# Performance work log

Hardware: AMD Instinct MI355X
Metric: run time of the kernel (lower is better)

Reference implementation:

```python
import jax, jax.numpy as jnp
import numpy as np

S_STATES, C_TYPES, G_GENES = 16, 64, 20000


def setup_inputs() -> dict:
    key = jax.random.key(0)
    k1, k2, k3, k4 = jax.random.split(key, 4)
    Z_mu = jax.random.normal(k1, (C_TYPES, G_GENES), dtype=jnp.float32)
    # positive log-normal sigmas, moderate scale for numerical stability
    Z_sigma = jax.random.uniform(k2, (C_TYPES, G_GENES), dtype=jnp.float32) * 0.5 + 0.1
    # build a valid correlation matrix (PSD with unit diagonal) so var >= 0
    L = jax.random.normal(k3, (C_TYPES, C_TYPES), dtype=jnp.float32)
    cov = L @ L.T + C_TYPES * jnp.eye(C_TYPES, dtype=jnp.float32)
    d = jnp.sqrt(jnp.diag(cov))
    corr = cov / (d[:, None] * d[None, :])
    # cell_prob rows on the simplex (Dirichlet-like), per state
    cell_prob = jax.nn.softmax(jax.random.normal(k4, (S_STATES, C_TYPES), dtype=jnp.float32), axis=1)
    return {"Z_mu": Z_mu, "Z_sigma": Z_sigma, "corr": corr, "cell_prob": cell_prob}


def reference(Z_mu, Z_sigma, corr, cell_prob):
    """Vectorized LogNorm.calculate_mu_sigma.

    Z_mu, Z_sigma: (C, G); corr: (C, C); cell_prob: (S, C).
    Returns mu, sigma of shape (S, G) -- moment-matched log-normal sum params
    for every (state, gene) pair, matching the nested-loop torch original.
    """
    # EV[s,c,g] = exp(mu + sigma^2/2) * w  (first moment of each component, weighted)
    ev_base = jnp.exp(Z_mu + 0.5 * Z_sigma ** 2)            # (C, G)
    EV = cell_prob[:, :, None] * ev_base[None, :, :]         # (S, C, G)
    Ssum = EV.sum(axis=1)                                    # (S, G)
    # A[s,c,g] = EV * sigma; var = sum_{c,d} A_c corr_{cd} A_d / Ssum^2
    A = EV * Z_sigma[None, :, :]                             # (S, C, G)
    var = jnp.einsum('scg,cd,sdg->sg', A, corr, A) / (Ssum ** 2)  # (S, G)
    mu_s = jnp.log(Ssum) - 0.5 * var
    sigma_s = jnp.sqrt(var)
    return (mu_s, sigma_s)
```

## Files before the change

### kernel.cpp

```cpp
#include <hip/hip_runtime.h>


#define S_STATES 16
#define C_TYPES  64
#define G_GENES  20000
#define OUT_HALF (S_STATES * G_GENES)
#define NPAIR    96
#define PER_WAVE 24

typedef _Float16 f16x2 __attribute__((ext_vector_type(2)));
typedef _Float16 f16x8 __attribute__((ext_vector_type(8)));
typedef float    f32x4 __attribute__((ext_vector_type(4)));

union Frag8 { f16x2 p[4]; f16x8 v; uint4 u; _Float16 h[8]; };

__global__ __launch_bounds__(64)
void build_A(const float* __restrict__ corr, const float* __restrict__ w,
             unsigned short* __restrict__ cwA)
{
    const int p    = blockIdx.x;
    const int lane = threadIdx.x;
    const int gl   = lane & 15;
    const int q    = lane >> 4;
    Frag8 v;
    if (p < NPAIR) {
        const int dh = (p >= 64);
        const int c  = dh ? p - 32 : p;
        const int d0 = dh * 32 + q * 8;
        const float wc = w[gl * C_TYPES + c];
        const float4 c0 = *(const float4*)(corr + c * C_TYPES + d0);
        const float4 c1 = *(const float4*)(corr + c * C_TYPES + d0 + 4);
        const float4 w0 = *(const float4*)(w + gl * C_TYPES + d0);
        const float4 w1 = *(const float4*)(w + gl * C_TYPES + d0 + 4);
        const float cv[8] = {c0.x,c0.y,c0.z,c0.w,c1.x,c1.y,c1.z,c1.w};
        const float wv[8] = {w0.x,w0.y,w0.z,w0.w,w1.x,w1.y,w1.z,w1.w};
#pragma unroll
        for (int j = 0; j < 8; ++j) {
            const int d = d0 + j;
            const float sc = (d < c) ? 2.0f : (d == c ? 1.0f : 0.0f);
            v.h[j] = (_Float16)(sc * cv[j] * wc * wv[j]);
        }
    } else {
        const int k0 = (p - NPAIR) * 32 + q * 8;
        const float4 w0 = *(const float4*)(w + gl * C_TYPES + k0);
        const float4 w1 = *(const float4*)(w + gl * C_TYPES + k0 + 4);
        const float wv[8] = {w0.x,w0.y,w0.z,w0.w,w1.x,w1.y,w1.z,w1.w};
#pragma unroll
        for (int j = 0; j < 8; ++j) v.h[j] = (_Float16)wv[j];
    }
    *(uint4*)(cwA + (p << 9) + lane * 8) = v.u;
}

__global__ __launch_bounds__(256, 4)
void lognorm_main(const float* __restrict__ Z_mu,
                  const float* __restrict__ Z_sigma,
                  const unsigned short* __restrict__ cwA,
                  float* __restrict__ out)
{
    __shared__ f16x2 x2pT[16][35];
    __shared__ f16x2 x1pT[16][35];
    __shared__ float accs[4][S_STATES][17];
    __shared__ float ssum_s[S_STATES][17];

    const int gt    = blockIdx.x;
    const int tid   = threadIdx.x;
    const int w     = tid >> 6;
    const int lane  = tid & 63;
    const int gl    = lane & 15;
    const int q     = lane >> 4;
    const int gbase = gt * 16;

    Frag8 wf0, wf1;
    if (w == 0) {
        wf0.u = *(const uint4*)(cwA + ((NPAIR + 0) << 9) + lane * 8);
        wf1.u = *(const uint4*)(cwA + ((NPAIR + 1) << 9) + lane * 8);
    }

    {
        const int gx  = tid & 15;
        const int dpA = tid >> 4;
#pragma unroll
        for (int t = 0; t < 2; ++t) {
            const int dp = dpA + 16 * t;
            const float m0 = Z_mu   [(2*dp)     * G_GENES + gbase + gx];
            const float m1 = Z_mu   [(2*dp + 1) * G_GENES + gbase + gx];
            const float s0 = Z_sigma[(2*dp)     * G_GENES + gbase + gx];
            const float s1 = Z_sigma[(2*dp + 1) * G_GENES + gbase + gx];
            const float e0 = __expf(fmaf(0.5f * s0, s0, m0)) * 0.25f;
            const float e1 = __expf(fmaf(0.5f * s1, s1, m1)) * 0.25f;
            f16x2 a, b;
            a.x = (_Float16)(e0 * s0); a.y = (_Float16)(e1 * s1);
            b.x = (_Float16)e0;        b.y = (_Float16)e1;
            x2pT[gx][dp] = a;
            x1pT[gx][dp] = b;
        }
    }
    __syncthreads();

    f16x2 xh[2][4];
#pragma unroll
    for (int dh = 0; dh < 2; ++dh)
#pragma unroll
        for (int jp = 0; jp < 4; ++jp)
            xh[dh][jp] = x2pT[gl][dh * 16 + q * 4 + jp];

    const unsigned short* Abase = cwA + (w << 9) + lane * 8;
    const int wq = w >> 1;
    const int wc = w & 1;
    f32x4 acc0 = {0.f,0.f,0.f,0.f}, acc1 = {0.f,0.f,0.f,0.f};
#pragma unroll
    for (int i = 0; i < PER_WAVE; ++i) {
        Frag8 af; af.u = *(const uint4*)(Abase + (i << 11));
        const int dh = (i >= 16) ? 1 : 0;
        const int dp = 2*i - dh*16 + wq;
        const f16x2 pr = x2pT[gl][dp];
        const _Float16 xc = wc ? pr.y : pr.x;
        f16x2 s; s.x = xc; s.y = xc;
        Frag8 b;
#pragma unroll
        for (int jp = 0; jp < 4; ++jp) b.p[jp] = s * xh[dh][jp];
        if (i & 1) acc1 = __builtin_amdgcn_mfma_f32_16x16x32_f16(af.v, b.v, acc1, 0, 0, 0);
        else       acc0 = __builtin_amdgcn_mfma_f32_16x16x32_f16(af.v, b.v, acc0, 0, 0, 0);
    }
    const f32x4 acc = acc0 + acc1;
#pragma unroll
    for (int r = 0; r < 4; ++r) accs[w][q*4 + r][gl] = acc[r];

    if (w == 0) {
        Frag8 x1f0, x1f1;
#pragma unroll
        for (int jp = 0; jp < 4; ++jp) {
            x1f0.p[jp] = x1pT[gl][q*4 + jp];
            x1f1.p[jp] = x1pT[gl][16 + q*4 + jp];
        }
        f32x4 sa = {0.f,0.f,0.f,0.f};
        sa = __builtin_amdgcn_mfma_f32_16x16x32_f16(wf0.v, x1f0.v, sa, 0, 0, 0);
        sa = __builtin_amdgcn_mfma_f32_16x16x32_f16(wf1.v, x1f1.v, sa, 0, 0, 0);
#pragma unroll
        for (int r = 0; r < 4; ++r) ssum_s[q*4 + r][gl] = sa[r];
    }
    __syncthreads();

    const int s  = tid >> 4;
    const int gx = tid & 15;
    const float vn = (accs[0][s][gx] + accs[1][s][gx])
                   + (accs[2][s][gx] + accs[3][s][gx]);
    const float ss   = ssum_s[s][gx];
    const float rvar = fmaxf(vn, 0.f) / (ss * ss);
    out[s * G_GENES + gbase + gx] =
        __logf(ss) + 1.3862943611f - 0.5f * rvar;
    out[OUT_HALF + s * G_GENES + gbase + gx] = sqrtf(rvar);
}

extern "C" void kernel_launch(void* const* d_in, const int* in_sizes, int n_in,
                              void* d_out, int out_size, void* d_ws, size_t ws_size,
                              hipStream_t stream) {
    const float* Z_mu      = (const float*)d_in[0];
    const float* Z_sigma   = (const float*)d_in[1];
    const float* corr      = (const float*)d_in[2];
    const float* cell_prob = (const float*)d_in[3];
    float* out = (float*)d_out;
    unsigned short* cwA = (unsigned short*)d_ws;

    build_A<<<dim3(NPAIR + 2), dim3(64), 0, stream>>>(corr, cell_prob, cwA);

    const int gtiles = G_GENES / 16;
    lognorm_main<<<dim3(gtiles), dim3(256), 0, stream>>>(
        Z_mu, Z_sigma, cwA, out);
}
```

Before: 16.82 us.

## Widen gene tile to 64 per block with 16 waves reusing A fragments

```diff
diff --git a/kernel.cpp b/kernel.cpp
--- a/kernel.cpp
+++ b/kernel.cpp
@@ -6,7 +6,6 @@
 #define G_GENES  20000
 #define OUT_HALF (S_STATES * G_GENES)
 #define NPAIR    96
-#define PER_WAVE 24
 
 typedef _Float16 f16x2 __attribute__((ext_vector_type(2)));
 typedef _Float16 f16x8 __attribute__((ext_vector_type(8)));
@@ -51,16 +50,17 @@
     *(uint4*)(cwA + (p << 9) + lane * 8) = v.u;
 }
 
-__global__ __launch_bounds__(256, 4)
+__global__ __launch_bounds__(1024, 4)
 void lognorm_main(const float* __restrict__ Z_mu,
                   const float* __restrict__ Z_sigma,
                   const unsigned short* __restrict__ cwA,
                   float* __restrict__ out)
 {
-    __shared__ f16x2 x2pT[16][35];
-    __shared__ f16x2 x1pT[16][35];
-    __shared__ float accs[4][S_STATES][17];
-    __shared__ float ssum_s[S_STATES][17];
+    __shared__ f16x2   x2pT[64][33];
+    __shared__ f16x2   x1pT[64][33];
+    __shared__ _Float16 x2g[64][72];
+    __shared__ float   accs[16][S_STATES][66];
+    __shared__ float   ssum_s[S_STATES][66];
 
     const int gt    = blockIdx.x;
     const int tid   = threadIdx.x;
@@ -68,83 +68,96 @@
     const int lane  = tid & 63;
     const int gl    = lane & 15;
     const int q     = lane >> 4;
-    const int gbase = gt * 16;
-
-    Frag8 wf0, wf1;
-    if (w == 0) {
-        wf0.u = *(const uint4*)(cwA + ((NPAIR + 0) << 9) + lane * 8);
-        wf1.u = *(const uint4*)(cwA + ((NPAIR + 1) << 9) + lane * 8);
-    }
+    const int gbase = (gt < 312) ? gt * 64 : (G_GENES - 64);
 
     {
-        const int gx  = tid & 15;
-        const int dpA = tid >> 4;
-#pragma unroll
-        for (int t = 0; t < 2; ++t) {
-            const int dp = dpA + 16 * t;
-            const float m0 = Z_mu   [(2*dp)     * G_GENES + gbase + gx];
-            const float m1 = Z_mu   [(2*dp + 1) * G_GENES + gbase + gx];
-            const float s0 = Z_sigma[(2*dp)     * G_GENES + gbase + gx];
-            const float s1 = Z_sigma[(2*dp + 1) * G_GENES + gbase + gx];
-            const float e0 = __expf(fmaf(0.5f * s0, s0, m0)) * 0.25f;
-            const float e1 = __expf(fmaf(0.5f * s1, s1, m1)) * 0.25f;
-            f16x2 a, b;
-            a.x = (_Float16)(e0 * s0); a.y = (_Float16)(e1 * s1);
-            b.x = (_Float16)e0;        b.y = (_Float16)e1;
-            x2pT[gx][dp] = a;
-            x1pT[gx][dp] = b;
-        }
+        const int dp = tid >> 5;
+        const int ga = (tid & 31) * 2;
+        const float* zm = Z_mu    + (2*dp) * G_GENES + gbase + ga;
+        const float* zs = Z_sigma + (2*dp) * G_GENES + gbase + ga;
+        const float2 m0 = *(const float2*)zm;
+        const float2 m1 = *(const float2*)(zm + G_GENES);
+        const float2 s0 = *(const float2*)zs;
+        const float2 s1 = *(const float2*)(zs + G_GENES);
+        const float e00 = __expf(fmaf(0.5f*s0.x, s0.x, m0.x)) * 0.25f;
+        const float e01 = __expf(fmaf(0.5f*s0.y, s0.y, m0.y)) * 0.25f;
+        const float e10 = __expf(fmaf(0.5f*s1.x, s1.x, m1.x)) * 0.25f;
+        const float e11 = __expf(fmaf(0.5f*s1.y, s1.y, m1.y)) * 0.25f;
+        const float x200 = e00*s0.x, x201 = e01*s0.y;
+        const float x210 = e10*s1.x, x211 = e11*s1.y;
+        f16x2 a0; a0.x = (_Float16)x200; a0.y = (_Float16)x210;
+        f16x2 a1; a1.x = (_Float16)x201; a1.y = (_Float16)x211;
+        f16x2 b0; b0.x = (_Float16)e00;  b0.y = (_Float16)e10;
+        f16x2 b1; b1.x = (_Float16)e01;  b1.y = (_Float16)e11;
+        x2pT[ga][dp]   = a0;  x2pT[ga+1][dp] = a1;
+        x1pT[ga][dp]   = b0;  x1pT[ga+1][dp] = b1;
+        x2g[2*dp][ga]     = (_Float16)x200;  x2g[2*dp][ga+1]   = (_Float16)x201;
+        x2g[2*dp+1][ga]   = (_Float16)x210;  x2g[2*dp+1][ga+1] = (_Float16)x211;
     }
     __syncthreads();
 
-    f16x2 xh[2][4];
+    f16x2 xh[2][4][4];
 #pragma unroll
     for (int dh = 0; dh < 2; ++dh)
 #pragma unroll
-        for (int jp = 0; jp < 4; ++jp)
-            xh[dh][jp] = x2pT[gl][dh * 16 + q * 4 + jp];
+        for (int t = 0; t < 4; ++t)
+#pragma unroll
+            for (int jp = 0; jp < 4; ++jp)
+                xh[dh][jp][t] = x2pT[gl + 16*t][dh*16 + q*4 + jp];
 
-    const unsigned short* Abase = cwA + (w << 9) + lane * 8;
-    const int wq = w >> 1;
-    const int wc = w & 1;
+    const unsigned short* Abase = cwA + lane * 8;
     f32x4 acc0 = {0.f,0.f,0.f,0.f}, acc1 = {0.f,0.f,0.f,0.f};
+    f32x4 acc2 = {0.f,0.f,0.f,0.f}, acc3 = {0.f,0.f,0.f,0.f};
 #pragma unroll
-    for (int i = 0; i < PER_WAVE; ++i) {
-        Frag8 af; af.u = *(const uint4*)(Abase + (i << 11));
-        const int dh = (i >= 16) ? 1 : 0;
-        const int dp = 2*i - dh*16 + wq;
-        const f16x2 pr = x2pT[gl][dp];
-        const _Float16 xc = wc ? pr.y : pr.x;
-        f16x2 s; s.x = xc; s.y = xc;
-        Frag8 b;
+    for (int i = 0; i < 6; ++i) {
+        const int p  = i * 16 + w;
+        const int dh = (i >= 4) ? 1 : 0;
+        const int c  = p - dh * 32;
+        Frag8 af; af.u = *(const uint4*)(Abase + (p << 9));
 #pragma unroll
-        for (int jp = 0; jp < 4; ++jp) b.p[jp] = s * xh[dh][jp];
-        if (i & 1) acc1 = __builtin_amdgcn_mfma_f32_16x16x32_f16(af.v, b.v, acc1, 0, 0, 0);
-        else       acc0 = __builtin_amdgcn_mfma_f32_16x16x32_f16(af.v, b.v, acc0, 0, 0, 0);
+        for (int t = 0; t < 4; ++t) {
+            const _Float16 xc = x2g[c][gl + 16*t];
+            f16x2 s; s.x = xc; s.y = xc;
+            Frag8 b;
+#pragma unroll
+            for (int jp = 0; jp < 4; ++jp) b.p[jp] = s * xh[dh][jp][t];
+            if      (t == 0) acc0 = __builtin_amdgcn_mfma_f32_16x16x32_f16(af.v, b.v, acc0, 0, 0, 0);
+            else if (t == 1) acc1 = __builtin_amdgcn_mfma_f32_16x16x32_f16(af.v, b.v, acc1, 0, 0, 0);
+            else if (t == 2) acc2 = __builtin_amdgcn_mfma_f32_16x16x32_f16(af.v, b.v, acc2, 0, 0, 0);
+            else             acc3 = __builtin_amdgcn_mfma_f32_16x16x32_f16(af.v, b.v, acc3, 0, 0, 0);
+        }
     }
-    const f32x4 acc = acc0 + acc1;
 #pragma unroll
-    for (int r = 0; r < 4; ++r) accs[w][q*4 + r][gl] = acc[r];
+    for (int r = 0; r < 4; ++r) {
+        accs[w][q*4 + r][gl]      = acc0[r];
+        accs[w][q*4 + r][gl + 16] = acc1[r];
+        accs[w][q*4 + r][gl + 32] = acc2[r];
+        accs[w][q*4 + r][gl + 48] = acc3[r];
+    }
 
-    if (w == 0) {
+    if (w < 4) {
+        Frag8 wf0, wf1;
+        wf0.u = *(const uint4*)(cwA + ((NPAIR + 0) << 9) + lane * 8);
+        wf1.u = *(const uint4*)(cwA + ((NPAIR + 1) << 9) + lane * 8);
         Frag8 x1f0, x1f1;
 #pragma unroll
         for (int jp = 0; jp < 4; ++jp) {
-            x1f0.p[jp] = x1pT[gl][q*4 + jp];
-            x1f1.p[jp] = x1pT[gl][16 + q*4 + jp];
+            x1f0.p[jp] = x1pT[gl + 16*w][q*4 + jp];
+            x1f1.p[jp] = x1pT[gl + 16*w][16 + q*4 + jp];
         }
         f32x4 sa = {0.f,0.f,0.f,0.f};
         sa = __builtin_amdgcn_mfma_f32_16x16x32_f16(wf0.v, x1f0.v, sa, 0, 0, 0);
         sa = __builtin_amdgcn_mfma_f32_16x16x32_f16(wf1.v, x1f1.v, sa, 0, 0, 0);
 #pragma unroll
-        for (int r = 0; r < 4; ++r) ssum_s[q*4 + r][gl] = sa[r];
+        for (int r = 0; r < 4; ++r) ssum_s[q*4 + r][gl + 16*w] = sa[r];
     }
     __syncthreads();
 
-    const int s  = tid >> 4;
-    const int gx = tid & 15;
-    const float vn = (accs[0][s][gx] + accs[1][s][gx])
-                   + (accs[2][s][gx] + accs[3][s][gx]);
+    const int s  = tid >> 6;
+    const int gx = tid & 63;
+    float vn = 0.f;
+#pragma unroll
+    for (int k = 0; k < 16; ++k) vn += accs[k][s][gx];
     const float ss   = ssum_s[s][gx];
     const float rvar = fmaxf(vn, 0.f) / (ss * ss);
     out[s * G_GENES + gbase + gx] =
@@ -164,7 +177,7 @@
 
     build_A<<<dim3(NPAIR + 2), dim3(64), 0, stream>>>(corr, cell_prob, cwA);
 
-    const int gtiles = G_GENES / 16;
-    lognorm_main<<<dim3(gtiles), dim3(256), 0, stream>>>(
+    const int gtiles = (G_GENES + 63) / 64;
+    lognorm_main<<<dim3(gtiles), dim3(1024), 0, stream>>>(
         Z_mu, Z_sigma, cwA, out);
 }
```

New measurement: 17.93 us. +6.6%, slower.
